# Kernel optimization log

Measured on AMD Instinct MI355X. Metric: run time of the kernel, lower is better.

Reference implementation:

```python
import jax, jax.numpy as jnp
import numpy as np

N_SRC = 50000
N_DST = 50000
N_EDGES = 500000
HIDDEN = 128
HEADS = 8
HEAD_DIM = HIDDEN // HEADS
SCALE = HEAD_DIM ** -0.5


def setup_inputs() -> dict:
    key = jax.random.key(0)
    ks = jax.random.split(key, 12)
    lim = 1.0 / np.sqrt(HIDDEN)
    def lin(k):
        kw, kb = jax.random.split(k)
        W = jax.random.uniform(kw, (HIDDEN, HIDDEN), jnp.float32, -lim, lim)
        b = jax.random.uniform(kb, (HIDDEN,), jnp.float32, -lim, lim)
        return W, b
    Wq, bq = lin(ks[0]); Wk, bk = lin(ks[1]); Wv, bv = lin(ks[2]); Wo, bo = lin(ks[3])
    return {
        "x_src": jax.random.normal(ks[4], (N_SRC, HIDDEN), jnp.float32),
        "x_dst": jax.random.normal(ks[5], (N_DST, HIDDEN), jnp.float32),
        "edge_index": jax.random.randint(ks[6], (2, N_EDGES), 0, N_SRC, jnp.int64),
        "Wq": Wq, "bq": bq, "Wk": Wk, "bk": bk, "Wv": Wv, "bv": bv,
        "Wo": Wo, "bo": bo,
        "edge_bias": jax.random.normal(ks[7], (HEADS,), jnp.float32) * 0.02,
    }


def reference(x_src, x_dst, edge_index, Wq, bq, Wk, bk, Wv, bv, Wo, bo, edge_bias):
    num_dst = x_dst.shape[0]
    # projections (torch Linear: y = x W^T + b), reshape to (N, H, D)
    q = (x_dst @ Wq.T + bq).reshape(num_dst, HEADS, HEAD_DIM)
    k = (x_src @ Wk.T + bk).reshape(-1, HEADS, HEAD_DIM)
    v = (x_src @ Wv.T + bv).reshape(-1, HEADS, HEAD_DIM)
    src_idx, dst_idx = edge_index[0], edge_index[1]
    # per-edge dot-product scores: (E, H)
    scores = (q[dst_idx] * k[src_idx]).sum(-1) * SCALE + edge_bias
    # sparse softmax over edges grouped by destination
    m = jax.ops.segment_max(scores, dst_idx, num_segments=num_dst)  # (N_dst, H)
    e = jnp.exp(scores - m[dst_idx])
    s = jax.ops.segment_sum(e, dst_idx, num_segments=num_dst)  # (N_dst, H)
    w = e / (s[dst_idx] + 1e-8)  # (E, H)
    # scatter-add aggregate weighted values
    out = jax.ops.segment_sum(w[:, :, None] * v[src_idx], dst_idx, num_segments=num_dst)
    out = out.reshape(num_dst, HIDDEN)
    return out @ Wo.T + bo
```

## Files before the change

kernel.cpp:

```cpp
#include <hip/hip_runtime.h>
#include <math.h>

#define HIDDEN 128
#define SCALE 0.25f
#define NB_TYPE 170
#define NB_O 256

typedef __attribute__((ext_vector_type(8))) short short8v;
typedef __attribute__((ext_vector_type(4))) float f32x4;

__device__ __forceinline__ unsigned short f2bf(float f) {
  const unsigned u = __float_as_uint(f);
  const unsigned r = u + 0x7fffu + ((u >> 16) & 1u);
  return (unsigned short)(r >> 16);
}
__device__ __forceinline__ unsigned pack_bf2(float a, float b) {
  unsigned r;
  asm("v_cvt_pk_bf16_f32 %0, %1, %2" : "=v"(r) : "v"(a), "v"(b));
  return r;
}
__device__ __forceinline__ float bflo(unsigned u) { return __uint_as_float(u << 16); }
__device__ __forceinline__ float bfhi(unsigned u) { return __uint_as_float(u & 0xffff0000u); }

__device__ __forceinline__ void gload_lds16(const void* g, void* l) {
  __builtin_amdgcn_global_load_lds(
      (const __attribute__((address_space(1))) unsigned*)g,
      (__attribute__((address_space(3))) unsigned*)l, 16, 0, 0);
}

__global__ __launch_bounds__(256) void prep_kernel(
    const float* __restrict__ W0, const float* __restrict__ W1,
    const float* __restrict__ W2, const float* __restrict__ W3,
    unsigned short* __restrict__ Wfrag,
    const int* __restrict__ ei, int E, int* __restrict__ counts)
{
  if (blockIdx.x < 32) {
    const int chunk = blockIdx.x * 256 + threadIdx.x;
    const int m = chunk >> 11;
    const int rem = chunk & 2047;
    const int l = rem & 63;
    const int nkk = rem >> 6;
    const int n = nkk >> 2, kk = nkk & 3;
    const float* W = (m == 0) ? W0 : (m == 1) ? W1 : (m == 2) ? W2 : W3;
    const int row = n * 16 + (l & 15);
    const int k0 = kk * 32 + (l >> 4) * 8;
    const float4 v0 = *(const float4*)&W[row * 128 + k0];
    const float4 v1 = *(const float4*)&W[row * 128 + k0 + 4];
    uint4 o;
    o.x = (unsigned)f2bf(v0.x) | ((unsigned)f2bf(v0.y) << 16);
    o.y = (unsigned)f2bf(v0.z) | ((unsigned)f2bf(v0.w) << 16);
    o.z = (unsigned)f2bf(v1.x) | ((unsigned)f2bf(v1.y) << 16);
    o.w = (unsigned)f2bf(v1.z) | ((unsigned)f2bf(v1.w) << 16);
    *(uint4*)&Wfrag[(size_t)chunk * 8] = o;
  } else {
    const int e = ((blockIdx.x - 32) * 256 + threadIdx.x) * 4;
    if (e + 4 <= E) {
      const int4 d = *(const int4*)&ei[E + e];
      atomicAdd(&counts[d.x], 1);
      atomicAdd(&counts[d.y], 1);
      atomicAdd(&counts[d.z], 1);
      atomicAdd(&counts[d.w], 1);
    } else {
      for (int k = e; k < E; ++k) atomicAdd(&counts[ei[E + k]], 1);
    }
  }
}

__global__ __launch_bounds__(256, 2) void qkv_gemm_kernel(
    const float* __restrict__ x_src, const float* __restrict__ x_dst,
    const unsigned short* __restrict__ Wfrag,
    const float* __restrict__ bq, const float* __restrict__ bk,
    const float* __restrict__ bv,
    unsigned short* __restrict__ qb, unsigned short* __restrict__ kvb,
    int Nsrc, int Ndst)
{
  __shared__ __align__(16) char Xs[2][16384];
  const int t = threadIdx.x;
  const int l = t & 63, w = t >> 6;
  const int r16 = l & 15, g16 = l >> 4;

  int bid = blockIdx.x;
  const float* X; const float* bias; const unsigned short* wbase;
  unsigned short* out; int ostride, ooff, N;
  if (bid < NB_TYPE)          { X = x_src; bias = bk; wbase = Wfrag + 16384; out = kvb; ostride = 256; ooff = 0;   N = Nsrc; }
  else if (bid < 2 * NB_TYPE) { bid -= NB_TYPE;   X = x_src; bias = bv; wbase = Wfrag + 32768; out = kvb; ostride = 256; ooff = 128; N = Nsrc; }
  else                        { bid -= 2 * NB_TYPE; X = x_dst; bias = bq; wbase = Wfrag;       out = qb;  ostride = 128; ooff = 0;   N = Ndst; }
  const int ntiles = (N + 63) >> 6;

  short8v wfr[32];
  #pragma unroll
  for (int i = 0; i < 32; ++i) wfr[i] = ((const short8v*)wbase)[i * 64 + l];

  const int srow = l >> 5;
  const int scol = (l & 31) * 4;

  float4 xv[8];
  int tile = bid;
  {
    #pragma unroll
    for (int j = 0; j < 8; ++j) {
      const int r = j * 2 + srow;
      const int g = tile * 64 + w * 16 + r;
      xv[j] = make_float4(0.f, 0.f, 0.f, 0.f);
      if (g < N) xv[j] = *(const float4*)&X[(size_t)g * 128 + scol];
    }
    #pragma unroll
    for (int j = 0; j < 8; ++j) {
      const int r = j * 2 + srow;
      uint2 p;
      p.x = pack_bf2(xv[j].x, xv[j].y);
      p.y = pack_bf2(xv[j].z, xv[j].w);
      *(uint2*)&Xs[0][(w * 16 + r) * 256 + ((scol * 2) ^ ((r & 7) << 4))] = p;
    }
  }
  int cur = 0;
  for (; tile < ntiles; tile += NB_TYPE) {
    const int nt = tile + NB_TYPE;
    if (nt < ntiles) {
      #pragma unroll
      for (int j = 0; j < 8; ++j) {
        const int r = j * 2 + srow;
        const int g = nt * 64 + w * 16 + r;
        xv[j] = make_float4(0.f, 0.f, 0.f, 0.f);
        if (g < N) xv[j] = *(const float4*)&X[(size_t)g * 128 + scol];
      }
    }
    f32x4 acc[8];
    #pragma unroll
    for (int n = 0; n < 8; ++n) {
      const float4 bb = *(const float4*)&bias[n * 16 + g16 * 4];
      acc[n] = (f32x4){bb.x, bb.y, bb.z, bb.w};
    }
    const char* ax = &Xs[cur][(w * 16 + r16) * 256];
    #pragma unroll
    for (int kk = 0; kk < 4; ++kk) {
      const short8v b = *(const short8v*)(ax + ((kk * 64 + g16 * 16) ^ ((r16 & 7) << 4)));
      #pragma unroll
      for (int n = 0; n < 8; ++n)
        acc[n] = __builtin_amdgcn_mfma_f32_16x16x32_bf16(wfr[n * 4 + kk], b, acc[n], 0, 0, 0);
    }
    const int grow = tile * 64 + w * 16 + r16;
    if (grow < N) {
      unsigned short* orow = out + (size_t)grow * ostride + ooff;
      #pragma unroll
      for (int n = 0; n < 8; ++n) {
        uint2 o;
        o.x = pack_bf2(acc[n][0], acc[n][1]);
        o.y = pack_bf2(acc[n][2], acc[n][3]);
        *(uint2*)&orow[n * 16 + g16 * 4] = o;
      }
    }
    if (nt < ntiles) {
      #pragma unroll
      for (int j = 0; j < 8; ++j) {
        const int r = j * 2 + srow;
        uint2 p;
        p.x = pack_bf2(xv[j].x, xv[j].y);
        p.y = pack_bf2(xv[j].z, xv[j].w);
        *(uint2*)&Xs[cur ^ 1][(w * 16 + r) * 256 + ((scol * 2) ^ ((r & 7) << 4))] = p;
      }
    }
    cur ^= 1;
  }
}

__global__ __launch_bounds__(256, 2) void out_gemm_kernel(
    const unsigned short* __restrict__ agg, const unsigned short* __restrict__ Wo_frag,
    const float* __restrict__ bo, float* __restrict__ Y, int N)
{
  __shared__ __align__(16) char Xs[2][16384];
  const int t = threadIdx.x;
  const int l = t & 63, w = t >> 6;
  const int r16 = l & 15, g16 = l >> 4;
  const int ntiles = (N + 63) >> 6;

  short8v wfr[32];
  #pragma unroll
  for (int i = 0; i < 32; ++i) wfr[i] = ((const short8v*)Wo_frag)[i * 64 + l];

  int tile = blockIdx.x;
  {
    #pragma unroll
    for (int it = 0; it < 4; ++it) {
      const int row16 = it * 4 + (l >> 4);
      const int grow = tile * 64 + w * 16 + row16;
      const int sb = ((l & 15) * 16) ^ ((row16 & 7) << 4);
      gload_lds16((const char*)agg + (size_t)grow * 256 + sb,
                  &Xs[0][w * 4096 + it * 1024 + l * 16]);
    }
  }
  int cur = 0;
  for (; tile < ntiles; tile += NB_O) {
    const int nt = tile + NB_O;
    asm volatile("s_waitcnt vmcnt(0)" ::: "memory");
    __builtin_amdgcn_sched_barrier(0);
    if (nt < ntiles) {
      #pragma unroll
      for (int it = 0; it < 4; ++it) {
        const int row16 = it * 4 + (l >> 4);
        const int grow = nt * 64 + w * 16 + row16;
        const int sb = ((l & 15) * 16) ^ ((row16 & 7) << 4);
        gload_lds16((const char*)agg + (size_t)grow * 256 + sb,
                    &Xs[cur ^ 1][w * 4096 + it * 1024 + l * 16]);
      }
    }
    f32x4 acc[8];
    #pragma unroll
    for (int n = 0; n < 8; ++n) {
      const float4 bb = *(const float4*)&bo[n * 16 + g16 * 4];
      acc[n] = (f32x4){bb.x, bb.y, bb.z, bb.w};
    }
    const char* ax = &Xs[cur][(w * 16 + r16) * 256];
    #pragma unroll
    for (int kk = 0; kk < 4; ++kk) {
      const short8v b = *(const short8v*)(ax + ((kk * 64 + g16 * 16) ^ ((r16 & 7) << 4)));
      #pragma unroll
      for (int n = 0; n < 8; ++n)
        acc[n] = __builtin_amdgcn_mfma_f32_16x16x32_bf16(wfr[n * 4 + kk], b, acc[n], 0, 0, 0);
    }
    const int grow = tile * 64 + w * 16 + r16;
    if (grow < N) {
      float* yrow = Y + (size_t)grow * 128;
      #pragma unroll
      for (int n = 0; n < 8; ++n)
        *(float4*)&yrow[n * 16 + g16 * 4] = make_float4(acc[n][0], acc[n][1], acc[n][2], acc[n][3]);
    }
    cur ^= 1;
  }
}

__global__ __launch_bounds__(256) void reduce_counts_kernel(
    const int* __restrict__ counts, int n, int* __restrict__ bsums)
{
  const int idx = blockIdx.x * 256 + threadIdx.x;
  int x = (idx < n) ? counts[idx] : 0;
  #pragma unroll
  for (int off = 1; off < 64; off <<= 1) x += __shfl_xor(x, off);
  __shared__ int ws[4];
  if ((threadIdx.x & 63) == 0) ws[threadIdx.x >> 6] = x;
  __syncthreads();
  if (threadIdx.x == 0) bsums[blockIdx.x] = ws[0] + ws[1] + ws[2] + ws[3];
}

__global__ __launch_bounds__(256) void scan_bsums_kernel(int* bsums, int nb)
{
  __shared__ int buf[256];
  const int t = threadIdx.x;
  const int x = (t < nb) ? bsums[t] : 0;
  buf[t] = x;
  __syncthreads();
  int val = x;
  #pragma unroll
  for (int off = 1; off < 256; off <<= 1) {
    const int other = (t >= off) ? buf[t - off] : 0;
    __syncthreads();
    val += other;
    buf[t] = val;
    __syncthreads();
  }
  if (t < nb) bsums[t] = val - x;
}

__global__ __launch_bounds__(256) void scan_counts_kernel(
    const int* __restrict__ counts, int n, const int* __restrict__ bsums,
    int* __restrict__ offsets)
{
  const int idx = blockIdx.x * 256 + threadIdx.x;
  const int lane = threadIdx.x & 63, wid = threadIdx.x >> 6;
  const int x = (idx < n) ? counts[idx] : 0;
  int v = x;
  #pragma unroll
  for (int off = 1; off < 64; off <<= 1) {
    const int t2 = __shfl_up(v, off);
    if (lane >= off) v += t2;
  }
  __shared__ int wsum[4];
  if (lane == 63) wsum[wid] = v;
  __syncthreads();
  int wbase = 0;
  for (int p = 0; p < wid; ++p) wbase += wsum[p];
  if (idx < n) offsets[idx] = bsums[blockIdx.x] + wbase + v - x;
}

__global__ __launch_bounds__(256) void scatter_kernel(
    const int* __restrict__ ei, int E, const int* __restrict__ offsets,
    int* __restrict__ cursor, int* __restrict__ csr_src)
{
  const int e = (blockIdx.x * 256 + threadIdx.x) * 4;
  if (e + 4 <= E) {
    const int4 s = *(const int4*)&ei[e];
    const int4 d = *(const int4*)&ei[E + e];
    int p;
    p = atomicAdd(&cursor[d.x], 1); csr_src[offsets[d.x] + p] = s.x;
    p = atomicAdd(&cursor[d.y], 1); csr_src[offsets[d.y] + p] = s.y;
    p = atomicAdd(&cursor[d.z], 1); csr_src[offsets[d.z] + p] = s.z;
    p = atomicAdd(&cursor[d.w], 1); csr_src[offsets[d.w] + p] = s.w;
  } else {
    for (int k = e; k < E; ++k) {
      const int d = ei[E + k];
      const int p = atomicAdd(&cursor[d], 1);
      csr_src[offsets[d] + p] = ei[k];
    }
  }
}

__global__ __launch_bounds__(256) void edge_attn_kernel(
    const unsigned short* __restrict__ qb, const unsigned short* __restrict__ kvb,
    const float* __restrict__ eb, const int* __restrict__ offsets,
    const int* __restrict__ counts, const int* __restrict__ csr_src,
    unsigned short* __restrict__ agg, int Ndst)
{
  const int wave = blockIdx.x * 4 + (threadIdx.x >> 6);
  if (wave >= Ndst) return;
  const int lane = threadIdx.x & 63;
  const int eg = lane >> 3, h = lane & 7;

  const uint4 q0 = *(const uint4*)&qb[(size_t)wave * 128 + h * 16];
  const uint4 q1 = *(const uint4*)&qb[(size_t)wave * 128 + h * 16 + 8];
  const float bias = eb[h];
  const int ro = offsets[wave];
  const int cnt = counts[wave];

  float acc[16];
  #pragma unroll
  for (int j = 0; j < 16; ++j) acc[j] = 0.f;
  float s = 0.f;

  for (int it = 0; it * 8 < cnt; ++it) {
    const int e = it * 8 + eg;
    const bool act = e < cnt;
    const int src = act ? csr_src[ro + e] : 0;
    const size_t base = (size_t)src * 256 + h * 16;
    const uint4 k0 = *(const uint4*)&kvb[base];
    const uint4 k1 = *(const uint4*)&kvb[base + 8];
    const uint4 v0 = *(const uint4*)&kvb[base + 128];
    const uint4 v1 = *(const uint4*)&kvb[base + 136];

    float p = 0.f;
    p = fmaf(bflo(q0.x), bflo(k0.x), p); p = fmaf(bfhi(q0.x), bfhi(k0.x), p);
    p = fmaf(bflo(q0.y), bflo(k0.y), p); p = fmaf(bfhi(q0.y), bfhi(k0.y), p);
    p = fmaf(bflo(q0.z), bflo(k0.z), p); p = fmaf(bfhi(q0.z), bfhi(k0.z), p);
    p = fmaf(bflo(q0.w), bflo(k0.w), p); p = fmaf(bfhi(q0.w), bfhi(k0.w), p);
    p = fmaf(bflo(q1.x), bflo(k1.x), p); p = fmaf(bfhi(q1.x), bfhi(k1.x), p);
    p = fmaf(bflo(q1.y), bflo(k1.y), p); p = fmaf(bfhi(q1.y), bfhi(k1.y), p);
    p = fmaf(bflo(q1.z), bflo(k1.z), p); p = fmaf(bfhi(q1.z), bfhi(k1.z), p);
    p = fmaf(bflo(q1.w), bflo(k1.w), p); p = fmaf(bfhi(q1.w), bfhi(k1.w), p);

    const float wgt = act ? __expf(fmaf(p, SCALE, bias)) : 0.f;
    s += wgt;
    acc[0]  = fmaf(wgt, bflo(v0.x), acc[0]);  acc[1]  = fmaf(wgt, bfhi(v0.x), acc[1]);
    acc[2]  = fmaf(wgt, bflo(v0.y), acc[2]);  acc[3]  = fmaf(wgt, bfhi(v0.y), acc[3]);
    acc[4]  = fmaf(wgt, bflo(v0.z), acc[4]);  acc[5]  = fmaf(wgt, bfhi(v0.z), acc[5]);
    acc[6]  = fmaf(wgt, bflo(v0.w), acc[6]);  acc[7]  = fmaf(wgt, bfhi(v0.w), acc[7]);
    acc[8]  = fmaf(wgt, bflo(v1.x), acc[8]);  acc[9]  = fmaf(wgt, bfhi(v1.x), acc[9]);
    acc[10] = fmaf(wgt, bflo(v1.y), acc[10]); acc[11] = fmaf(wgt, bfhi(v1.y), acc[11]);
    acc[12] = fmaf(wgt, bflo(v1.z), acc[12]); acc[13] = fmaf(wgt, bfhi(v1.z), acc[13]);
    acc[14] = fmaf(wgt, bflo(v1.w), acc[14]); acc[15] = fmaf(wgt, bfhi(v1.w), acc[15]);
  }

  #pragma unroll
  for (int m = 8; m <= 32; m <<= 1) {
    s += __shfl_xor(s, m);
    #pragma unroll
    for (int j = 0; j < 16; ++j) acc[j] += __shfl_xor(acc[j], m);
  }

  if (eg == 0) {
    const float rs = 1.0f / (s + 1e-8f);
    uint4 o0, o1;
    o0.x = pack_bf2(acc[0] * rs,  acc[1] * rs);
    o0.y = pack_bf2(acc[2] * rs,  acc[3] * rs);
    o0.z = pack_bf2(acc[4] * rs,  acc[5] * rs);
    o0.w = pack_bf2(acc[6] * rs,  acc[7] * rs);
    o1.x = pack_bf2(acc[8] * rs,  acc[9] * rs);
    o1.y = pack_bf2(acc[10] * rs, acc[11] * rs);
    o1.z = pack_bf2(acc[12] * rs, acc[13] * rs);
    o1.w = pack_bf2(acc[14] * rs, acc[15] * rs);
    *(uint4*)&agg[(size_t)wave * 128 + h * 16] = o0;
    *(uint4*)&agg[(size_t)wave * 128 + h * 16 + 8] = o1;
  }
}

extern "C" void kernel_launch(void* const* d_in, const int* in_sizes, int n_in,
                              void* d_out, int out_size, void* d_ws, size_t ws_size,
                              hipStream_t stream) {
  const float* x_src = (const float*)d_in[0];
  const float* x_dst = (const float*)d_in[1];
  const int*   ei    = (const int*)d_in[2];
  const float* Wq = (const float*)d_in[3];
  const float* bq = (const float*)d_in[4];
  const float* Wk = (const float*)d_in[5];
  const float* bk = (const float*)d_in[6];
  const float* Wv = (const float*)d_in[7];
  const float* bv = (const float*)d_in[8];
  const float* Wo = (const float*)d_in[9];
  const float* bo = (const float*)d_in[10];
  const float* eb = (const float*)d_in[11];

  const int Nsrc = in_sizes[0] / HIDDEN;
  const int Ndst = in_sizes[1] / HIDDEN;
  const int E    = in_sizes[2] / 2;

  char* w = (char*)d_ws;
  unsigned short* qb   = (unsigned short*)w; w += (size_t)Ndst * 128 * 2;
  unsigned short* kvb  = (unsigned short*)w; w += (size_t)Nsrc * 256 * 2;
  unsigned short* aggb = (unsigned short*)w; w += (size_t)Ndst * 128 * 2;
  unsigned short* Wb   = (unsigned short*)w; w += (size_t)4 * 16384 * 2;
  int* counts  = (int*)w; w += (size_t)Ndst * sizeof(int);
  int* cursor  = (int*)w; w += (size_t)Ndst * sizeof(int);
  int* offsets = (int*)w; w += (size_t)Ndst * sizeof(int);
  int* bsums   = (int*)w; w += 256 * sizeof(int);
  int* csr_src = (int*)w; w += (size_t)E * sizeof(int);

  hipMemsetAsync(counts, 0, (size_t)Ndst * 2 * sizeof(int), stream);

  dim3 blk256(256);
  const int e4blocks = (E / 4 + 255) / 256;
  prep_kernel<<<32 + e4blocks, blk256, 0, stream>>>(Wq, Wk, Wv, Wo, Wb, ei, E, counts);

  qkv_gemm_kernel<<<3 * NB_TYPE, blk256, 0, stream>>>(
      x_src, x_dst, Wb, bq, bk, bv, qb, kvb, Nsrc, Ndst);

  const int nb = (Ndst + 255) / 256;
  reduce_counts_kernel<<<nb, blk256, 0, stream>>>(counts, Ndst, bsums);
  scan_bsums_kernel<<<1, blk256, 0, stream>>>(bsums, nb);
  scan_counts_kernel<<<nb, blk256, 0, stream>>>(counts, Ndst, bsums, offsets);

  scatter_kernel<<<e4blocks, blk256, 0, stream>>>(ei, E, offsets, cursor, csr_src);

  const int ablocks = (Ndst + 3) / 4;
  edge_attn_kernel<<<ablocks, blk256, 0, stream>>>(qb, kvb, eb, offsets, counts,
                                                   csr_src, aggb, Ndst);

  out_gemm_kernel<<<NB_O, blk256, 0, stream>>>(aggb, Wb + 49152, bo, (float*)d_out, Ndst);
}
```

Measured before the change: 146.0 us.

## Split GEMM weights across waves, fuse count scan, prefetch CSR indices, reduce-scatter outputs

```diff
diff --git a/kernel.cpp b/kernel.cpp
--- a/kernel.cpp
+++ b/kernel.cpp
@@ -3,8 +3,7 @@
 
 #define HIDDEN 128
 #define SCALE 0.25f
-#define NB_TYPE 170
-#define NB_O 256
+#define NB_G 391
 
 typedef __attribute__((ext_vector_type(8))) short short8v;
 typedef __attribute__((ext_vector_type(4))) float f32x4;
@@ -66,7 +65,7 @@
   }
 }
 
-__global__ __launch_bounds__(256, 2) void qkv_gemm_kernel(
+__global__ __launch_bounds__(256, 4) void qkv_gemm_kernel(
     const float* __restrict__ x_src, const float* __restrict__ x_dst,
     const unsigned short* __restrict__ Wfrag,
     const float* __restrict__ bq, const float* __restrict__ bk,
@@ -82,90 +81,105 @@
   int bid = blockIdx.x;
   const float* X; const float* bias; const unsigned short* wbase;
   unsigned short* out; int ostride, ooff, N;
-  if (bid < NB_TYPE)          { X = x_src; bias = bk; wbase = Wfrag + 16384; out = kvb; ostride = 256; ooff = 0;   N = Nsrc; }
-  else if (bid < 2 * NB_TYPE) { bid -= NB_TYPE;   X = x_src; bias = bv; wbase = Wfrag + 32768; out = kvb; ostride = 256; ooff = 128; N = Nsrc; }
-  else                        { bid -= 2 * NB_TYPE; X = x_dst; bias = bq; wbase = Wfrag;       out = qb;  ostride = 128; ooff = 0;   N = Ndst; }
+  if (bid < NB_G)        { X = x_src; bias = bk; wbase = Wfrag + 16384; out = kvb; ostride = 256; ooff = 0;   N = Nsrc; }
+  else if (bid < 2*NB_G) { bid -= NB_G;   X = x_src; bias = bv; wbase = Wfrag + 32768; out = kvb; ostride = 256; ooff = 128; N = Nsrc; }
+  else                   { bid -= 2*NB_G; X = x_dst; bias = bq; wbase = Wfrag;         out = qb;  ostride = 128; ooff = 0;   N = Ndst; }
   const int ntiles = (N + 63) >> 6;
 
-  short8v wfr[32];
-  #pragma unroll
-  for (int i = 0; i < 32; ++i) wfr[i] = ((const short8v*)wbase)[i * 64 + l];
-
-  const int srow = l >> 5;
-  const int scol = (l & 31) * 4;
+  short8v wfr[2][4];
+  #pragma unroll
+  for (int cb = 0; cb < 2; ++cb)
+    #pragma unroll
+    for (int kk = 0; kk < 4; ++kk)
+      wfr[cb][kk] = ((const short8v*)wbase)[((w * 2 + cb) * 4 + kk) * 64 + l];
+  float4 bb[2];
+  #pragma unroll
+  for (int cb = 0; cb < 2; ++cb) bb[cb] = *(const float4*)&bias[w * 32 + cb * 16 + g16 * 4];
 
   float4 xv[8];
   int tile = bid;
   {
     #pragma unroll
-    for (int j = 0; j < 8; ++j) {
-      const int r = j * 2 + srow;
-      const int g = tile * 64 + w * 16 + r;
-      xv[j] = make_float4(0.f, 0.f, 0.f, 0.f);
-      if (g < N) xv[j] = *(const float4*)&X[(size_t)g * 128 + scol];
-    }
-    #pragma unroll
-    for (int j = 0; j < 8; ++j) {
-      const int r = j * 2 + srow;
+    for (int it = 0; it < 8; ++it) {
+      const int c = it * 256 + t;
+      const int row = c >> 5, fc = (c & 31) << 2;
+      const int g = tile * 64 + row;
+      xv[it] = make_float4(0.f, 0.f, 0.f, 0.f);
+      if (g < N) xv[it] = *(const float4*)&X[(size_t)g * 128 + fc];
+    }
+    #pragma unroll
+    for (int it = 0; it < 8; ++it) {
+      const int c = it * 256 + t;
+      const int row = c >> 5, b8 = (c & 31) << 3;
       uint2 p;
-      p.x = pack_bf2(xv[j].x, xv[j].y);
-      p.y = pack_bf2(xv[j].z, xv[j].w);
-      *(uint2*)&Xs[0][(w * 16 + r) * 256 + ((scol * 2) ^ ((r & 7) << 4))] = p;
-    }
-  }
+      p.x = pack_bf2(xv[it].x, xv[it].y);
+      p.y = pack_bf2(xv[it].z, xv[it].w);
+      *(uint2*)&Xs[0][row * 256 + (b8 ^ ((row & 7) << 4))] = p;
+    }
+    __syncthreads();
+  }
+
   int cur = 0;
-  for (; tile < ntiles; tile += NB_TYPE) {
-    const int nt = tile + NB_TYPE;
+  for (; tile < ntiles; tile += NB_G) {
+    const int nt = tile + NB_G;
     if (nt < ntiles) {
       #pragma unroll
-      for (int j = 0; j < 8; ++j) {
-        const int r = j * 2 + srow;
-        const int g = nt * 64 + w * 16 + r;
-        xv[j] = make_float4(0.f, 0.f, 0.f, 0.f);
-        if (g < N) xv[j] = *(const float4*)&X[(size_t)g * 128 + scol];
-      }
-    }
-    f32x4 acc[8];
-    #pragma unroll
-    for (int n = 0; n < 8; ++n) {
-      const float4 bb = *(const float4*)&bias[n * 16 + g16 * 4];
-      acc[n] = (f32x4){bb.x, bb.y, bb.z, bb.w};
-    }
-    const char* ax = &Xs[cur][(w * 16 + r16) * 256];
-    #pragma unroll
-    for (int kk = 0; kk < 4; ++kk) {
-      const short8v b = *(const short8v*)(ax + ((kk * 64 + g16 * 16) ^ ((r16 & 7) << 4)));
-      #pragma unroll
-      for (int n = 0; n < 8; ++n)
-        acc[n] = __builtin_amdgcn_mfma_f32_16x16x32_bf16(wfr[n * 4 + kk], b, acc[n], 0, 0, 0);
-    }
-    const int grow = tile * 64 + w * 16 + r16;
-    if (grow < N) {
-      unsigned short* orow = out + (size_t)grow * ostride + ooff;
-      #pragma unroll
-      for (int n = 0; n < 8; ++n) {
-        uint2 o;
-        o.x = pack_bf2(acc[n][0], acc[n][1]);
-        o.y = pack_bf2(acc[n][2], acc[n][3]);
-        *(uint2*)&orow[n * 16 + g16 * 4] = o;
+      for (int it = 0; it < 8; ++it) {
+        const int c = it * 256 + t;
+        const int row = c >> 5, fc = (c & 31) << 2;
+        const int g = nt * 64 + row;
+        xv[it] = make_float4(0.f, 0.f, 0.f, 0.f);
+        if (g < N) xv[it] = *(const float4*)&X[(size_t)g * 128 + fc];
+      }
+    }
+    f32x4 acc[4][2];
+    #pragma unroll
+    for (int rb = 0; rb < 4; ++rb)
+      #pragma unroll
+      for (int cb = 0; cb < 2; ++cb)
+        acc[rb][cb] = (f32x4){bb[cb].x, bb[cb].y, bb[cb].z, bb[cb].w};
+    #pragma unroll
+    for (int rb = 0; rb < 4; ++rb) {
+      const char* ax = &Xs[cur][(rb * 16 + r16) * 256];
+      #pragma unroll
+      for (int kk = 0; kk < 4; ++kk) {
+        const short8v b = *(const short8v*)(ax + (((kk * 32 + g16 * 8) * 2) ^ ((r16 & 7) << 4)));
+        acc[rb][0] = __builtin_amdgcn_mfma_f32_16x16x32_bf16(wfr[0][kk], b, acc[rb][0], 0, 0, 0);
+        acc[rb][1] = __builtin_amdgcn_mfma_f32_16x16x32_bf16(wfr[1][kk], b, acc[rb][1], 0, 0, 0);
+      }
+    }
+    #pragma unroll
+    for (int rb = 0; rb < 4; ++rb) {
+      const int g = tile * 64 + rb * 16 + r16;
+      if (g < N) {
+        unsigned short* orow = out + (size_t)g * ostride + ooff + w * 32;
+        #pragma unroll
+        for (int cb = 0; cb < 2; ++cb) {
+          uint2 o;
+          o.x = pack_bf2(acc[rb][cb][0], acc[rb][cb][1]);
+          o.y = pack_bf2(acc[rb][cb][2], acc[rb][cb][3]);
+          *(uint2*)&orow[cb * 16 + g16 * 4] = o;
+        }
       }
     }
     if (nt < ntiles) {
       #pragma unroll
-      for (int j = 0; j < 8; ++j) {
-        const int r = j * 2 + srow;
+      for (int it = 0; it < 8; ++it) {
+        const int c = it * 256 + t;
+        const int row = c >> 5, b8 = (c & 31) << 3;
         uint2 p;
-        p.x = pack_bf2(xv[j].x, xv[j].y);
-        p.y = pack_bf2(xv[j].z, xv[j].w);
-        *(uint2*)&Xs[cur ^ 1][(w * 16 + r) * 256 + ((scol * 2) ^ ((r & 7) << 4))] = p;
-      }
-    }
+        p.x = pack_bf2(xv[it].x, xv[it].y);
+        p.y = pack_bf2(xv[it].z, xv[it].w);
+        *(uint2*)&Xs[cur ^ 1][row * 256 + (b8 ^ ((row & 7) << 4))] = p;
+      }
+    }
+    __syncthreads();
     cur ^= 1;
   }
 }
 
-__global__ __launch_bounds__(256, 2) void out_gemm_kernel(
-    const unsigned short* __restrict__ agg, const unsigned short* __restrict__ Wo_frag,
+__global__ __launch_bounds__(256, 4) void out_gemm_kernel(
+    const unsigned short* __restrict__ agg, const unsigned short* __restrict__ Wfrag_o,
     const float* __restrict__ bo, float* __restrict__ Y, int N)
 {
   __shared__ __align__(16) char Xs[2][16384];
@@ -174,112 +188,107 @@
   const int r16 = l & 15, g16 = l >> 4;
   const int ntiles = (N + 63) >> 6;
 
-  short8v wfr[32];
-  #pragma unroll
-  for (int i = 0; i < 32; ++i) wfr[i] = ((const short8v*)Wo_frag)[i * 64 + l];
+  short8v wfr[2][4];
+  #pragma unroll
+  for (int cb = 0; cb < 2; ++cb)
+    #pragma unroll
+    for (int kk = 0; kk < 4; ++kk)
+      wfr[cb][kk] = ((const short8v*)Wfrag_o)[((w * 2 + cb) * 4 + kk) * 64 + l];
+  float4 bb[2];
+  #pragma unroll
+  for (int cb = 0; cb < 2; ++cb) bb[cb] = *(const float4*)&bo[w * 32 + cb * 16 + g16 * 4];
 
   int tile = blockIdx.x;
-  {
-    #pragma unroll
-    for (int it = 0; it < 4; ++it) {
-      const int row16 = it * 4 + (l >> 4);
-      const int grow = tile * 64 + w * 16 + row16;
-      const int sb = ((l & 15) * 16) ^ ((row16 & 7) << 4);
-      gload_lds16((const char*)agg + (size_t)grow * 256 + sb,
-                  &Xs[0][w * 4096 + it * 1024 + l * 16]);
-    }
+  #pragma unroll
+  for (int it = 0; it < 4; ++it) {
+    const int c = it * 256 + t;
+    const int row = c >> 4, c16 = c & 15;
+    gload_lds16((const char*)agg + (size_t)(tile * 64 + row) * 256 + ((c16 * 16) ^ ((row & 7) << 4)),
+                &Xs[0][c * 16]);
   }
   int cur = 0;
-  for (; tile < ntiles; tile += NB_O) {
-    const int nt = tile + NB_O;
+  for (; tile < ntiles; tile += NB_G) {
+    const int nt = tile + NB_G;
     asm volatile("s_waitcnt vmcnt(0)" ::: "memory");
     __builtin_amdgcn_sched_barrier(0);
+    __syncthreads();
     if (nt < ntiles) {
       #pragma unroll
       for (int it = 0; it < 4; ++it) {
-        const int row16 = it * 4 + (l >> 4);
-        const int grow = nt * 64 + w * 16 + row16;
-        const int sb = ((l & 15) * 16) ^ ((row16 & 7) << 4);
-        gload_lds16((const char*)agg + (size_t)grow * 256 + sb,
-                    &Xs[cur ^ 1][w * 4096 + it * 1024 + l * 16]);
-      }
-    }
-    f32x4 acc[8];
-    #pragma unroll
-    for (int n = 0; n < 8; ++n) {
-      const float4 bb = *(const float4*)&bo[n * 16 + g16 * 4];
-      acc[n] = (f32x4){bb.x, bb.y, bb.z, bb.w};
-    }
-    const char* ax = &Xs[cur][(w * 16 + r16) * 256];
-    #pragma unroll
-    for (int kk = 0; kk < 4; ++kk) {
-      const short8v b = *(const short8v*)(ax + ((kk * 64 + g16 * 16) ^ ((r16 & 7) << 4)));
-      #pragma unroll
-      for (int n = 0; n < 8; ++n)
-        acc[n] = __builtin_amdgcn_mfma_f32_16x16x32_bf16(wfr[n * 4 + kk], b, acc[n], 0, 0, 0);
-    }
-    const int grow = tile * 64 + w * 16 + r16;
-    if (grow < N) {
-      float* yrow = Y + (size_t)grow * 128;
-      #pragma unroll
-      for (int n = 0; n < 8; ++n)
-        *(float4*)&yrow[n * 16 + g16 * 4] = make_float4(acc[n][0], acc[n][1], acc[n][2], acc[n][3]);
+        const int c = it * 256 + t;
+        const int row = c >> 4, c16 = c & 15;
+        gload_lds16((const char*)agg + (size_t)(nt * 64 + row) * 256 + ((c16 * 16) ^ ((row & 7) << 4)),
+                    &Xs[cur ^ 1][c * 16]);
+      }
+    }
+    f32x4 acc[4][2];
+    #pragma unroll
+    for (int rb = 0; rb < 4; ++rb)
+      #pragma unroll
+      for (int cb = 0; cb < 2; ++cb)
+        acc[rb][cb] = (f32x4){bb[cb].x, bb[cb].y, bb[cb].z, bb[cb].w};
+    #pragma unroll
+    for (int rb = 0; rb < 4; ++rb) {
+      const char* ax = &Xs[cur][(rb * 16 + r16) * 256];
+      #pragma unroll
+      for (int kk = 0; kk < 4; ++kk) {
+        const short8v b = *(const short8v*)(ax + (((kk * 32 + g16 * 8) * 2) ^ ((r16 & 7) << 4)));
+        acc[rb][0] = __builtin_amdgcn_mfma_f32_16x16x32_bf16(wfr[0][kk], b, acc[rb][0], 0, 0, 0);
+        acc[rb][1] = __builtin_amdgcn_mfma_f32_16x16x32_bf16(wfr[1][kk], b, acc[rb][1], 0, 0, 0);
+      }
+    }
+    #pragma unroll
+    for (int rb = 0; rb < 4; ++rb) {
+      const int g = tile * 64 + rb * 16 + r16;
+      if (g < N) {
+        float* yrow = Y + (size_t)g * 128 + w * 32;
+        #pragma unroll
+        for (int cb = 0; cb < 2; ++cb)
+          *(float4*)&yrow[cb * 16 + g16 * 4] =
+              make_float4(acc[rb][cb][0], acc[rb][cb][1], acc[rb][cb][2], acc[rb][cb][3]);
+      }
     }
     cur ^= 1;
   }
 }
 
-__global__ __launch_bounds__(256) void reduce_counts_kernel(
-    const int* __restrict__ counts, int n, int* __restrict__ bsums)
-{
-  const int idx = blockIdx.x * 256 + threadIdx.x;
-  int x = (idx < n) ? counts[idx] : 0;
-  #pragma unroll
-  for (int off = 1; off < 64; off <<= 1) x += __shfl_xor(x, off);
-  __shared__ int ws[4];
-  if ((threadIdx.x & 63) == 0) ws[threadIdx.x >> 6] = x;
-  __syncthreads();
-  if (threadIdx.x == 0) bsums[blockIdx.x] = ws[0] + ws[1] + ws[2] + ws[3];
-}
-
-__global__ __launch_bounds__(256) void scan_bsums_kernel(int* bsums, int nb)
-{
-  __shared__ int buf[256];
-  const int t = threadIdx.x;
-  const int x = (t < nb) ? bsums[t] : 0;
-  buf[t] = x;
-  __syncthreads();
-  int val = x;
-  #pragma unroll
-  for (int off = 1; off < 256; off <<= 1) {
-    const int other = (t >= off) ? buf[t - off] : 0;
-    __syncthreads();
-    val += other;
-    buf[t] = val;
-    __syncthreads();
-  }
-  if (t < nb) bsums[t] = val - x;
-}
-
-__global__ __launch_bounds__(256) void scan_counts_kernel(
-    const int* __restrict__ counts, int n, const int* __restrict__ bsums,
-    int* __restrict__ offsets)
-{
-  const int idx = blockIdx.x * 256 + threadIdx.x;
-  const int lane = threadIdx.x & 63, wid = threadIdx.x >> 6;
+__global__ __launch_bounds__(256) void scan_fused_kernel(
+    const int* __restrict__ counts, int n, int* __restrict__ bsums,
+    int* __restrict__ done, int* __restrict__ offsets)
+{
+  const int b = blockIdx.x, t = threadIdx.x;
+  const int lane = t & 63, wid = t >> 6;
+  const int idx = b * 256 + t;
   const int x = (idx < n) ? counts[idx] : 0;
   int v = x;
   #pragma unroll
   for (int off = 1; off < 64; off <<= 1) {
-    const int t2 = __shfl_up(v, off);
-    if (lane >= off) v += t2;
+    const int tmp = __shfl_up(v, off);
+    if (lane >= off) v += tmp;
   }
   __shared__ int wsum[4];
+  __shared__ int base_s;
   if (lane == 63) wsum[wid] = v;
+  __syncthreads();
+  if (t == 0) {
+    bsums[b] = wsum[0] + wsum[1] + wsum[2] + wsum[3];
+    __threadfence();
+    atomicAdd(done, 1);
+    while (atomicAdd(done, 0) < (int)gridDim.x) {}
+  }
+  __syncthreads();
+  __threadfence();
+  int pre = (t < b) ? bsums[t] : 0;
+  #pragma unroll
+  for (int off = 1; off < 64; off <<= 1) pre += __shfl_xor(pre, off);
+  __shared__ int pres[4];
+  if (lane == 0) pres[wid] = pre;
+  __syncthreads();
+  if (t == 0) base_s = pres[0] + pres[1] + pres[2] + pres[3];
   __syncthreads();
   int wbase = 0;
   for (int p = 0; p < wid; ++p) wbase += wsum[p];
-  if (idx < n) offsets[idx] = bsums[blockIdx.x] + wbase + v - x;
+  if (idx < n) offsets[idx] = base_s + wbase + v - x;
 }
 
 __global__ __launch_bounds__(256) void scatter_kernel(
@@ -326,15 +335,19 @@
   for (int j = 0; j < 16; ++j) acc[j] = 0.f;
   float s = 0.f;
 
-  for (int it = 0; it * 8 < cnt; ++it) {
-    const int e = it * 8 + eg;
-    const bool act = e < cnt;
-    const int src = act ? csr_src[ro + e] : 0;
+  int e = eg;
+  bool act = e < cnt;
+  int src = act ? csr_src[ro + e] : 0;
+  const int iters = (cnt + 7) >> 3;
+  for (int it = 0; it < iters; ++it) {
     const size_t base = (size_t)src * 256 + h * 16;
     const uint4 k0 = *(const uint4*)&kvb[base];
     const uint4 k1 = *(const uint4*)&kvb[base + 8];
     const uint4 v0 = *(const uint4*)&kvb[base + 128];
     const uint4 v1 = *(const uint4*)&kvb[base + 136];
+    const int e2 = e + 8;
+    const bool act2 = e2 < cnt;
+    const int src2 = act2 ? csr_src[ro + e2] : 0;
 
     float p = 0.f;
     p = fmaf(bflo(q0.x), bflo(k0.x), p); p = fmaf(bfhi(q0.x), bfhi(k0.x), p);
@@ -356,29 +369,35 @@
     acc[10] = fmaf(wgt, bflo(v1.y), acc[10]); acc[11] = fmaf(wgt, bfhi(v1.y), acc[11]);
     acc[12] = fmaf(wgt, bflo(v1.z), acc[12]); acc[13] = fmaf(wgt, bfhi(v1.z), acc[13]);
     acc[14] = fmaf(wgt, bflo(v1.w), acc[14]); acc[15] = fmaf(wgt, bfhi(v1.w), acc[15]);
-  }
-
-  #pragma unroll
-  for (int m = 8; m <= 32; m <<= 1) {
-    s += __shfl_xor(s, m);
-    #pragma unroll
-    for (int j = 0; j < 16; ++j) acc[j] += __shfl_xor(acc[j], m);
-  }
-
-  if (eg == 0) {
-    const float rs = 1.0f / (s + 1e-8f);
-    uint4 o0, o1;
-    o0.x = pack_bf2(acc[0] * rs,  acc[1] * rs);
-    o0.y = pack_bf2(acc[2] * rs,  acc[3] * rs);
-    o0.z = pack_bf2(acc[4] * rs,  acc[5] * rs);
-    o0.w = pack_bf2(acc[6] * rs,  acc[7] * rs);
-    o1.x = pack_bf2(acc[8] * rs,  acc[9] * rs);
-    o1.y = pack_bf2(acc[10] * rs, acc[11] * rs);
-    o1.z = pack_bf2(acc[12] * rs, acc[13] * rs);
-    o1.w = pack_bf2(acc[14] * rs, acc[15] * rs);
-    *(uint4*)&agg[(size_t)wave * 128 + h * 16] = o0;
-    *(uint4*)&agg[(size_t)wave * 128 + h * 16 + 8] = o1;
-  }
+    e = e2; act = act2; src = src2;
+  }
+
+  const bool b0 = eg & 1, b1 = (eg >> 1) & 1, b2 = (eg >> 2) & 1;
+  float r8[8];
+  #pragma unroll
+  for (int j = 0; j < 8; ++j) {
+    const float keep = b0 ? acc[j + 8] : acc[j];
+    const float send = b0 ? acc[j] : acc[j + 8];
+    r8[j] = keep + __shfl_xor(send, 8);
+  }
+  float r4[4];
+  #pragma unroll
+  for (int j = 0; j < 4; ++j) {
+    const float keep = b1 ? r8[j + 4] : r8[j];
+    const float send = b1 ? r8[j] : r8[j + 4];
+    r4[j] = keep + __shfl_xor(send, 16);
+  }
+  float r2[2];
+  #pragma unroll
+  for (int j = 0; j < 2; ++j) {
+    const float keep = b2 ? r4[j + 2] : r4[j];
+    const float send = b2 ? r4[j] : r4[j + 2];
+    r2[j] = keep + __shfl_xor(send, 32);
+  }
+  s += __shfl_xor(s, 8); s += __shfl_xor(s, 16); s += __shfl_xor(s, 32);
+  const float rs = 1.0f / (s + 1e-8f);
+  const int col = h * 16 + (b0 ? 8 : 0) + (b1 ? 4 : 0) + (b2 ? 2 : 0);
+  *(unsigned*)&agg[(size_t)wave * 128 + col] = pack_bf2(r2[0] * rs, r2[1] * rs);
 }
 
 extern "C" void kernel_launch(void* const* d_in, const int* in_sizes, int n_in,
@@ -408,23 +427,22 @@
   unsigned short* Wb   = (unsigned short*)w; w += (size_t)4 * 16384 * 2;
   int* counts  = (int*)w; w += (size_t)Ndst * sizeof(int);
   int* cursor  = (int*)w; w += (size_t)Ndst * sizeof(int);
+  int* done    = (int*)w; w += 64 * sizeof(int);
   int* offsets = (int*)w; w += (size_t)Ndst * sizeof(int);
   int* bsums   = (int*)w; w += 256 * sizeof(int);
   int* csr_src = (int*)w; w += (size_t)E * sizeof(int);
 
-  hipMemsetAsync(counts, 0, (size_t)Ndst * 2 * sizeof(int), stream);
+  hipMemsetAsync(counts, 0, ((size_t)Ndst * 2 + 64) * sizeof(int), stream);
 
   dim3 blk256(256);
   const int e4blocks = (E / 4 + 255) / 256;
   prep_kernel<<<32 + e4blocks, blk256, 0, stream>>>(Wq, Wk, Wv, Wo, Wb, ei, E, counts);
 
-  qkv_gemm_kernel<<<3 * NB_TYPE, blk256, 0, stream>>>(
+  qkv_gemm_kernel<<<3 * NB_G, blk256, 0, stream>>>(
       x_src, x_dst, Wb, bq, bk, bv, qb, kvb, Nsrc, Ndst);
 
   const int nb = (Ndst + 255) / 256;
-  reduce_counts_kernel<<<nb, blk256, 0, stream>>>(counts, Ndst, bsums);
-  scan_bsums_kernel<<<1, blk256, 0, stream>>>(bsums, nb);
-  scan_counts_kernel<<<nb, blk256, 0, stream>>>(counts, Ndst, bsums, offsets);
+  scan_fused_kernel<<<nb, blk256, 0, stream>>>(counts, Ndst, bsums, done, offsets);
 
   scatter_kernel<<<e4blocks, blk256, 0, stream>>>(ei, E, offsets, cursor, csr_src);
 
@@ -432,5 +450,5 @@
   edge_attn_kernel<<<ablocks, blk256, 0, stream>>>(qb, kvb, eb, offsets, counts,
                                                    csr_src, aggb, Ndst);
 
-  out_gemm_kernel<<<NB_O, blk256, 0, stream>>>(aggb, Wb + 49152, bo, (float*)d_out, Ndst);
-}
+  out_gemm_kernel<<<NB_G, blk256, 0, stream>>>(aggb, Wb + 49152, bo, (float*)d_out, Ndst);
+}
```

Result: slower. 157.4 us (+7.8%).
